# Performance work log

Hardware: AMD Instinct MI355X
Metric: run time of the kernel (lower is better)

## Reference

```python
import jax, jax.numpy as jnp
import numpy as np

S, N, L, K = 64, 8192, 512, 128  # sentences, candidate spans, max sentence length, output spans


def setup_inputs() -> dict:
    key = jax.random.key(0)
    k1, k2, k3 = jax.random.split(key, 3)
    span_scores = jax.random.normal(k1, (S, N), dtype=jnp.float32)
    starts = jax.random.randint(k2, (S, N), 0, L - 30).astype(jnp.int32)
    widths = jax.random.randint(k3, (S, N), 0, 30).astype(jnp.int32)
    ends = jnp.minimum(starts + widths, L - 1)
    return {
        "span_scores": span_scores,
        "candidate_starts": starts,
        "candidate_ends": ends,
        "num_output_spans": K,
        "max_sentence_length": L,
    }


def _select_sentence(scores, starts, ends, num_out, max_len):
    # Greedy non-crossing span selection for one sentence.
    order = jnp.argsort(-scores).astype(jnp.int32)  # descending score order
    s_sorted = starts[order]
    e_sorted = ends[order]
    pos = jnp.arange(max_len, dtype=jnp.int32)

    def step(carry, x):
        s2e, e2s, sel, n = carry  # start->latest end (init -1), end->earliest start (init L)
        i, st, en = x
        # crossing iff exists j in (st, en] with latest_end[j] > en,
        #          or j in [st, en) with earliest_start[j] < st
        crossing = jnp.any(((pos > st) & (pos <= en) & (s2e > en))
                           | ((pos >= st) & (pos < en) & (e2s < st)))
        take = jnp.logical_and(jnp.logical_not(crossing), n < num_out)
        idx = jnp.minimum(n, num_out - 1)
        sel = sel.at[idx].set(jnp.where(take, i, sel[idx]))
        s2e = jnp.where(take, s2e.at[st].max(en), s2e)
        e2s = jnp.where(take, e2s.at[en].min(st), e2s)
        n = n + take.astype(jnp.int32)
        return (s2e, e2s, sel, n), None

    init = (jnp.full((max_len,), -1, jnp.int32),
            jnp.full((max_len,), max_len, jnp.int32),
            jnp.zeros((num_out,), jnp.int32),
            jnp.int32(0))
    (s2e, e2s, sel, n), _ = jax.lax.scan(step, init, (order, s_sorted, e_sorted))
    # pad unfilled slots with the first selected index (matches torch tail-fill)
    sel = jnp.where(jnp.arange(num_out) < n, sel, sel[0])
    # sort_spans=True: order selected spans by (start, end)
    keys = starts[sel] * max_len + ends[sel]
    sel = sel[jnp.argsort(keys)]
    return sel


def reference(span_scores, candidate_starts, candidate_ends, num_output_spans, max_sentence_length):
    f = jax.vmap(lambda s, cs, ce: _select_sentence(s, cs, ce, num_output_spans, max_sentence_length))
    return f(span_scores, candidate_starts, candidate_ends).astype(jnp.int32)
```

## Files before the change

### kernel.cpp

```cpp
#include <hip/hip_runtime.h>

#define NSENT 64
#define NCAND 8192
#define LMAX  512
#define KOUT  128
#define TPB   512
#define CHUNK 1024
#define NCHUNK (NCAND / CHUNK)

#if defined(__has_builtin)
#if __has_builtin(__builtin_amdgcn_readlane)
#define READLANE(v, l) __builtin_amdgcn_readlane((unsigned)(v), (unsigned)(l))
#endif
#endif
#ifndef READLANE
#define READLANE(v, l) ((unsigned)__shfl((int)(v), (int)(l)))
#endif

__global__ __launch_bounds__(TPB) void sort_chunks_kernel(
    const float* __restrict__ scores,
    const int*   __restrict__ starts,
    const int*   __restrict__ ends,
    unsigned long long* __restrict__ ws)
{
    __shared__ unsigned long long lk[CHUNK];
    const int  bid   = blockIdx.x;
    const int  sent  = bid >> 3;
    const int  chunk = bid & 7;
    const int  tid   = threadIdx.x;
    const long gbase = (long)sent * NCAND + (long)chunk * CHUNK;

    for (int i = tid; i < CHUNK; i += TPB) {
        unsigned u  = __float_as_uint(scores[gbase + i]);
        unsigned o  = (u & 0x80000000u) ? ~u : (u | 0x80000000u);
        unsigned d  = ~o;
        unsigned st = (unsigned)starts[gbase + i];
        unsigned en = (unsigned)ends[gbase + i];
        unsigned gi = (unsigned)(chunk * CHUNK + i);
        lk[i] = ((unsigned long long)d << 32) | (gi << 18) | (st << 9) | en;
    }

    for (int k = 2; k <= CHUNK; k <<= 1) {
        for (int j = k >> 1; j > 0; j >>= 1) {
            __syncthreads();
            const int p   = tid;
            const int low = p & (j - 1);
            const int i   = ((p - low) << 1) | low;
            const int q   = i | j;
            unsigned long long a = lk[i];
            unsigned long long b = lk[q];
            bool up = ((i & k) == 0);
            if ((a > b) == up) { lk[i] = b; lk[q] = a; }
        }
    }
    __syncthreads();

    unsigned long long* wo = ws + (long)bid * CHUNK;
    for (int i = tid; i < CHUNK; i += TPB) wo[i] = lk[i];
}

__global__ __launch_bounds__(TPB) void merge_kernel(
    unsigned long long* __restrict__ ws)
{
    __shared__ __align__(16) unsigned long long keys[NCAND];
    const int sent = blockIdx.x;
    const int tid  = threadIdx.x;
    unsigned long long* wi = ws + (long)sent * NCAND;

    {
        const ulonglong2* wi2 = (const ulonglong2*)wi;
        ulonglong2* k2 = (ulonglong2*)keys;
        for (int i = tid; i < NCAND / 2; i += TPB) k2[i] = wi2[i];
    }
    __syncthreads();

    #pragma unroll
    for (int stg = 0; stg < 3; ++stg) {
        const int Lh  = CHUNK << stg;
        const int tpp = Lh >> 3;
        const int pair = tid / tpp;
        const int o    = (tid % tpp) * 16;
        const unsigned long long* A = keys + pair * (Lh * 2);
        const unsigned long long* B = A + Lh;
        int lo = (o > Lh) ? o - Lh : 0;
        int hi = (o < Lh) ? o : Lh;
        while (lo < hi) {
            int mid = (lo + hi) >> 1;
            if (A[mid] <= B[o - 1 - mid]) lo = mid + 1; else hi = mid;
        }
        int i = lo, j = o - lo;
        unsigned long long r[16];
        #pragma unroll
        for (int x = 0; x < 16; ++x) {
            bool ta = (j >= Lh) || (i < Lh && A[i] <= B[j]);
            r[x] = ta ? A[i++] : B[j++];
        }
        __syncthreads();
        unsigned long long* O = keys + pair * (Lh * 2) + o;
        #pragma unroll
        for (int x = 0; x < 16; ++x) O[x] = r[x];
        __syncthreads();
    }

    {
        const ulonglong2* k2 = (const ulonglong2*)keys;
        ulonglong2* wo2 = (ulonglong2*)wi;
        for (int i = tid; i < NCAND / 2; i += TPB) wo2[i] = k2[i];
    }
}

__global__ __launch_bounds__(128) void greedy_kernel(
    const unsigned long long* __restrict__ ws,
    int* __restrict__ out)
{
    __shared__ int TT1[5][LMAX];
    __shared__ int TT2[5][LMAX];
    __shared__ unsigned acc_list[KOUT];
    __shared__ int      n_sh;
    __shared__ unsigned mkbuf[KOUT];
    __shared__ unsigned paybuf[KOUT];

    const int sent = blockIdx.x;
    const int tid  = threadIdx.x;
    const unsigned long long* wsp = ws + (long)sent * NCAND;

    for (int i = tid; i < 5 * LMAX; i += 128) {
        (&TT1[0][0])[i] = -1;
        (&TT2[0][0])[i] = LMAX;
    }
    __syncthreads();

    if (tid < 64) {
        const int lane = tid;
        const int sidel = (lane < 31) ? lane : (lane - 31);
        const int k_m   = 31 - __clz(sidel + 1);
        const int j_m   = sidel + 1 - (1 << k_m);
        int* const rowU = (lane < 31) ? &TT1[k_m][0] : &TT2[k_m][0];

        const int NW = NCAND / 64;
        unsigned long long kv0 = wsp[lane];
        unsigned long long kv1 = wsp[64 + lane];
        int n = 0;

        for (int w = 0; w < NW && n < KOUT; ++w) {
            const unsigned pay = (unsigned)kv0;
            kv0 = kv1;
            kv1 = (w + 2 < NW) ? wsp[(long)(w + 2) * 64 + lane] : 0ull;

            const int en = (int)(pay & 511u);
            const int st = (int)((pay >> 9) & 511u);
            const int wd = en - st;

            bool alive = true;
            if (wd > 0) {
                bool cross;
                if (wd < 32) {
                    const int k   = 31 - __clz(wd);
                    const int off = 1 << k;
                    const int mx  = max(TT1[k][st + 1], TT1[k][en + 1 - off]);
                    const int mn  = min(TT2[k][st],     TT2[k][en - off]);
                    cross = (mx > en) || (mn < st);
                } else {
                    cross = false;
                    for (int j = st; j <= en; ++j)
                        cross |= ((j > st) && (TT1[0][j] > en)) ||
                                 ((j < en) && (TT2[0][j] < st));
                }
                alive = !cross;
            }

            for (;;) {
                const unsigned long long anyb = __ballot((int)alive);
                if (anyb == 0ull) break;
                const int lwin = __ffsll((long long)anyb) - 1;
                const unsigned spay = READLANE(pay, lwin);
                const int sen = (int)(spay & 511u);
                const int sst = (int)((spay >> 9) & 511u);

                if (lane == 62) acc_list[n] = spay;
                if (lane < 31)      { const int i = sst - j_m; if (i >= 0) atomicMax(&rowU[i], sen); }
                else if (lane < 62) { const int i = sen - j_m; if (i >= 0) atomicMin(&rowU[i], sst); }
                if (lane == lwin) alive = false;
                ++n;
                if (n >= KOUT) break;
                const bool c = ((st < sst) & (sst <= en) & (sen > en)) |
                               ((sst < st) & (sen >= st) & (sen < en));
                alive = alive & !c;
            }
        }
        if (lane == 0) n_sh = n;
    }
    __syncthreads();

    const int n = n_sh;
    {
        const unsigned p = (tid < n) ? acc_list[tid] : acc_list[0];
        paybuf[tid] = p;
        mkbuf[tid]  = ((p & 0x3FFFFu) << 7) | (unsigned)tid;
    }
    __syncthreads();
    {
        const unsigned mk = mkbuf[tid];
        int r = 0;
        #pragma unroll 8
        for (int t2 = 0; t2 < KOUT; ++t2) r += (mkbuf[t2] < mk) ? 1 : 0;
        out[sent * KOUT + r] = (int)(paybuf[tid] >> 18);
    }
}

__global__ __launch_bounds__(TPB) void extract_spans_mono(
    const float* __restrict__ scores,
    const int*   __restrict__ starts,
    const int*   __restrict__ ends,
    int*         __restrict__ out)
{
    __shared__ unsigned long long keys[NCAND];
    __shared__ unsigned acc_list[KOUT];
    __shared__ unsigned long long amask[TPB/64];
    __shared__ unsigned mkbuf[KOUT];
    __shared__ unsigned paybuf[KOUT];

    const int  sent = blockIdx.x;
    const int  tid  = threadIdx.x;
    const long base = (long)sent * NCAND;

    for (int i = tid; i < NCAND; i += TPB) {
        unsigned u = __float_as_uint(scores[base + i]);
        unsigned o = (u & 0x80000000u) ? ~u : (u | 0x80000000u);
        unsigned d = ~o;
        unsigned st = (unsigned)starts[base + i];
        unsigned en = (unsigned)ends[base + i];
        keys[i] = ((unsigned long long)d << 32) | ((unsigned)i << 18) | (st << 9) | en;
    }
    for (int k = 2; k <= NCAND; k <<= 1) {
        for (int j = k >> 1; j > 0; j >>= 1) {
            __syncthreads();
            for (int p = tid; p < NCAND / 2; p += TPB) {
                int low = p & (j - 1);
                int i   = ((p - low) << 1) | low;
                int q   = i | j;
                unsigned long long a = keys[i];
                unsigned long long b = keys[q];
                bool up = ((i & k) == 0);
                if ((a > b) == up) { keys[i] = b; keys[q] = a; }
            }
        }
    }
    __syncthreads();

    int  nn   = 0;
    bool done = false;
    for (int cb = 0; cb < NCAND && !done; cb += TPB) {
        const unsigned pay = (unsigned)keys[cb + tid];
        const int en = (int)(pay & 511u);
        const int st = (int)((pay >> 9) & 511u);
        bool alive = true;
        for (int a = 0; a < nn; ++a) {
            unsigned ap = acc_list[a];
            int ae = (int)(ap & 511u), as = (int)((ap >> 9) & 511u);
            if ((st < as && as <= en && ae > en) || (as < st && ae >= st && ae < en)) {
                alive = false; break;
            }
        }
        for (;;) {
            unsigned long long m = __ballot((int)alive);
            if ((tid & 63) == 0) amask[tid >> 6] = m;
            __syncthreads();
            int s = -1;
            #pragma unroll
            for (int w = 0; w < TPB / 64; ++w) {
                unsigned long long mw = amask[w];
                if (s < 0 && mw) s = (w << 6) + __ffsll((long long)mw) - 1;
            }
            __syncthreads();
            if (s < 0) break;
            unsigned spay = (unsigned)keys[cb + s];
            int sen = (int)(spay & 511u), sst = (int)((spay >> 9) & 511u);
            if (tid == 0) acc_list[nn] = spay;
            ++nn;
            if (nn == KOUT) { done = true; break; }
            if (alive) {
                alive = (tid != s) &&
                        !((st < sst && sst <= en && sen > en) ||
                          (sst < st && sen >= st && sen < en));
            }
        }
    }
    __syncthreads();
    if (tid < KOUT) {
        unsigned pay = (tid < nn) ? acc_list[tid] : acc_list[0];
        paybuf[tid] = pay;
        mkbuf[tid]  = ((pay & 0x3FFFFu) << 7) | (unsigned)tid;
    }
    __syncthreads();
    if (tid < KOUT) {
        unsigned mk = mkbuf[tid];
        int rank = 0;
        for (int t2 = 0; t2 < KOUT; ++t2)
            rank += (mkbuf[t2] < mk) ? 1 : 0;
        out[sent * KOUT + rank] = (int)(paybuf[tid] >> 18);
    }
}

extern "C" void kernel_launch(void* const* d_in, const int* in_sizes, int n_in,
                              void* d_out, int out_size, void* d_ws, size_t ws_size,
                              hipStream_t stream) {
    const float* scores = (const float*)d_in[0];
    const int*   starts = (const int*)d_in[1];
    const int*   ends   = (const int*)d_in[2];
    int*         out    = (int*)d_out;

    const size_t ws_needed = (size_t)NSENT * NCAND * sizeof(unsigned long long);
    if (ws_size >= ws_needed) {
        unsigned long long* ws = (unsigned long long*)d_ws;
        sort_chunks_kernel<<<NSENT * NCHUNK, TPB, 0, stream>>>(scores, starts, ends, ws);
        merge_kernel<<<NSENT, TPB, 0, stream>>>(ws);
        greedy_kernel<<<NSENT, 128, 0, stream>>>(ws, out);
    } else {
        extract_spans_mono<<<NSENT, TPB, 0, stream>>>(scores, starts, ends, out);
    }
}
```

Measured before the change: 124.0 us.

## Fuse merge and greedy kernels, register-resident bitonic sort, prefetch next-wave crossing tables

The chunk sort now keeps two keys per thread in registers and uses wave shuffles for small strides, a register compare for stride 512, and double-buffered LDS exchanges only for mid strides. The merge and greedy kernels are fused so the greedy scan reads merged keys straight from LDS instead of writing them to global memory and reading them back. The greedy loop also software-pipelines the next wave's sparse-table lookups and tracks crossings against newly accepted spans incrementally. The intent is to cut global round-trips, one launch, and per-step barrier and latency cost. The trade-off is higher LDS use per block and a fused block where 448 threads sit idle during the greedy phase.

After: 130.3 us. 5.1% more time.

```diff
diff --git a/kernel.cpp b/kernel.cpp
--- a/kernel.cpp
+++ b/kernel.cpp
@@ -23,50 +23,82 @@
     const int*   __restrict__ ends,
     unsigned long long* __restrict__ ws)
 {
-    __shared__ unsigned long long lk[CHUNK];
+    __shared__ unsigned long long lb[2][CHUNK];
     const int  bid   = blockIdx.x;
     const int  sent  = bid >> 3;
     const int  chunk = bid & 7;
-    const int  tid   = threadIdx.x;
+    const int  t     = threadIdx.x;
     const long gbase = (long)sent * NCAND + (long)chunk * CHUNK;
 
-    for (int i = tid; i < CHUNK; i += TPB) {
-        unsigned u  = __float_as_uint(scores[gbase + i]);
-        unsigned o  = (u & 0x80000000u) ? ~u : (u | 0x80000000u);
-        unsigned d  = ~o;
-        unsigned st = (unsigned)starts[gbase + i];
-        unsigned en = (unsigned)ends[gbase + i];
-        unsigned gi = (unsigned)(chunk * CHUNK + i);
-        lk[i] = ((unsigned long long)d << 32) | (gi << 18) | (st << 9) | en;
-    }
-
+    unsigned long long a, b;
+    {
+        unsigned u0 = __float_as_uint(scores[gbase + t]);
+        unsigned u1 = __float_as_uint(scores[gbase + t + 512]);
+        unsigned o0 = (u0 & 0x80000000u) ? ~u0 : (u0 | 0x80000000u);
+        unsigned o1 = (u1 & 0x80000000u) ? ~u1 : (u1 | 0x80000000u);
+        unsigned st0 = (unsigned)starts[gbase + t];
+        unsigned st1 = (unsigned)starts[gbase + t + 512];
+        unsigned en0 = (unsigned)ends[gbase + t];
+        unsigned en1 = (unsigned)ends[gbase + t + 512];
+        unsigned g0 = (unsigned)(chunk * CHUNK + t);
+        unsigned g1 = (unsigned)(chunk * CHUNK + t + 512);
+        a = ((unsigned long long)(~o0) << 32) | (g0 << 18) | (st0 << 9) | en0;
+        b = ((unsigned long long)(~o1) << 32) | (g1 << 18) | (st1 << 9) | en1;
+    }
+
+    int cur = 0;
     for (int k = 2; k <= CHUNK; k <<= 1) {
         for (int j = k >> 1; j > 0; j >>= 1) {
-            __syncthreads();
-            const int p   = tid;
-            const int low = p & (j - 1);
-            const int i   = ((p - low) << 1) | low;
-            const int q   = i | j;
-            unsigned long long a = lk[i];
-            unsigned long long b = lk[q];
-            bool up = ((i & k) == 0);
-            if ((a > b) == up) { lk[i] = b; lk[q] = a; }
-        }
-    }
-    __syncthreads();
+            const bool upa = ((t & k) == 0);
+            const bool upb = (((t + 512) & k) == 0);
+            if (j == 512) {
+                unsigned long long lo = (a < b) ? a : b;
+                unsigned long long hi = (a < b) ? b : a;
+                a = lo; b = hi;
+            } else if (j >= 64) {
+                lb[cur][t] = a; lb[cur][t + 512] = b;
+                __syncthreads();
+                const unsigned long long pa = lb[cur][t ^ j];
+                const unsigned long long pb = lb[cur][(t ^ j) + 512];
+                cur ^= 1;
+                const bool low = ((t & j) == 0);
+                a = ((low == upa) == (a < pa)) ? a : pa;
+                b = ((low == upb) == (b < pb)) ? b : pb;
+            } else {
+                const unsigned long long pa = __shfl_xor(a, j);
+                const unsigned long long pb = __shfl_xor(b, j);
+                const bool low = ((t & j) == 0);
+                a = ((low == upa) == (a < pa)) ? a : pa;
+                b = ((low == upb) == (b < pb)) ? b : pb;
+            }
+        }
+    }
 
     unsigned long long* wo = ws + (long)bid * CHUNK;
-    for (int i = tid; i < CHUNK; i += TPB) wo[i] = lk[i];
+    wo[t]       = a;
+    wo[t + 512] = b;
 }
 
-__global__ __launch_bounds__(TPB) void merge_kernel(
-    unsigned long long* __restrict__ ws)
+__global__ __launch_bounds__(TPB) void merge_greedy_kernel(
+    const unsigned long long* __restrict__ ws,
+    int* __restrict__ out)
 {
     __shared__ __align__(16) unsigned long long keys[NCAND];
+    __shared__ int TT1[5][LMAX];
+    __shared__ int TT2[5][LMAX];
+    __shared__ unsigned acc_list[KOUT];
+    __shared__ int      n_sh;
+    __shared__ unsigned mkbuf[KOUT];
+    __shared__ unsigned paybuf[KOUT];
+
     const int sent = blockIdx.x;
     const int tid  = threadIdx.x;
-    unsigned long long* wi = ws + (long)sent * NCAND;
-
+    const unsigned long long* wi = ws + (long)sent * NCAND;
+
+    for (int i = tid; i < 5 * LMAX; i += TPB) {
+        (&TT1[0][0])[i] = -1;
+        (&TT2[0][0])[i] = LMAX;
+    }
     {
         const ulonglong2* wi2 = (const ulonglong2*)wi;
         ulonglong2* k2 = (ulonglong2*)keys;
@@ -102,104 +134,105 @@
         __syncthreads();
     }
 
-    {
-        const ulonglong2* k2 = (const ulonglong2*)keys;
-        ulonglong2* wo2 = (ulonglong2*)wi;
-        for (int i = tid; i < NCAND / 2; i += TPB) wo2[i] = k2[i];
-    }
-}
-
-__global__ __launch_bounds__(128) void greedy_kernel(
-    const unsigned long long* __restrict__ ws,
-    int* __restrict__ out)
-{
-    __shared__ int TT1[5][LMAX];
-    __shared__ int TT2[5][LMAX];
-    __shared__ unsigned acc_list[KOUT];
-    __shared__ int      n_sh;
-    __shared__ unsigned mkbuf[KOUT];
-    __shared__ unsigned paybuf[KOUT];
-
-    const int sent = blockIdx.x;
-    const int tid  = threadIdx.x;
-    const unsigned long long* wsp = ws + (long)sent * NCAND;
-
-    for (int i = tid; i < 5 * LMAX; i += 128) {
-        (&TT1[0][0])[i] = -1;
-        (&TT2[0][0])[i] = LMAX;
-    }
-    __syncthreads();
-
     if (tid < 64) {
         const int lane = tid;
         const int sidel = (lane < 31) ? lane : (lane - 31);
         const int k_m   = 31 - __clz(sidel + 1);
         const int j_m   = sidel + 1 - (1 << k_m);
         int* const rowU = (lane < 31) ? &TT1[k_m][0] : &TT2[k_m][0];
+        const unsigned* kw = (const unsigned*)keys;
 
         const int NW = NCAND / 64;
-        unsigned long long kv0 = wsp[lane];
-        unsigned long long kv1 = wsp[64 + lane];
+        unsigned payA = kw[(0 * 64 + lane) << 1];
+        unsigned payB = kw[(1 * 64 + lane) << 1];
+        int enA = (int)(payA & 511u), stA = (int)((payA >> 9) & 511u);
+        int enB = (int)(payB & 511u), stB = (int)((payB >> 9) & 511u);
+
+        bool aliveA;
+        {
+            const int wd = enA - stA;
+            bool cross = false;
+            if (wd > 0) {
+                if (wd < 32) {
+                    const int k = 31 - __clz(wd), off = 1 << k;
+                    const int mx = max(TT1[k][stA + 1], TT1[k][enA + 1 - off]);
+                    const int mn = min(TT2[k][stA],     TT2[k][enA - off]);
+                    cross = (mx > enA) || (mn < stA);
+                } else {
+                    for (int j = stA; j <= enA; ++j)
+                        cross |= ((j > stA) && (TT1[0][j] > enA)) ||
+                                 ((j < enA) && (TT2[0][j] < stA));
+                }
+            }
+            aliveA = !cross;
+        }
+        bool aliveBacc = true;
         int n = 0;
 
         for (int w = 0; w < NW && n < KOUT; ++w) {
-            const unsigned pay = (unsigned)kv0;
-            kv0 = kv1;
-            kv1 = (w + 2 < NW) ? wsp[(long)(w + 2) * 64 + lane] : 0ull;
-
-            const int en = (int)(pay & 511u);
-            const int st = (int)((pay >> 9) & 511u);
-            const int wd = en - st;
-
-            bool alive = true;
-            if (wd > 0) {
-                bool cross;
-                if (wd < 32) {
-                    const int k   = 31 - __clz(wd);
-                    const int off = 1 << k;
-                    const int mx  = max(TT1[k][st + 1], TT1[k][en + 1 - off]);
-                    const int mn  = min(TT2[k][st],     TT2[k][en - off]);
-                    cross = (mx > en) || (mn < st);
-                } else {
-                    cross = false;
-                    for (int j = st; j <= en; ++j)
-                        cross |= ((j > st) && (TT1[0][j] > en)) ||
-                                 ((j < en) && (TT2[0][j] < st));
-                }
-                alive = !cross;
-            }
+            const int wdB = enB - stB;
+            int kB = (wdB >= 1) ? (31 - __clz(wdB)) : 0;
+            if (kB > 4) kB = 4;
+            const int offB = 1 << kB;
+            int ia = stB + 1;        if (ia > 511) ia = 511;
+            int ib = enB + 1 - offB; if (ib < 0)   ib = 0;
+            const int ic = stB;
+            int id = enB - offB;     if (id < 0)   id = 0;
+            const int tA = TT1[kB][ia], tB = TT1[kB][ib];
+            const int tC = TT2[kB][ic], tD = TT2[kB][id];
 
             for (;;) {
-                const unsigned long long anyb = __ballot((int)alive);
+                const unsigned long long anyb = __ballot((int)aliveA);
                 if (anyb == 0ull) break;
                 const int lwin = __ffsll((long long)anyb) - 1;
-                const unsigned spay = READLANE(pay, lwin);
+                const unsigned spay = READLANE(payA, lwin);
                 const int sen = (int)(spay & 511u);
                 const int sst = (int)((spay >> 9) & 511u);
 
                 if (lane == 62) acc_list[n] = spay;
                 if (lane < 31)      { const int i = sst - j_m; if (i >= 0) atomicMax(&rowU[i], sen); }
                 else if (lane < 62) { const int i = sen - j_m; if (i >= 0) atomicMin(&rowU[i], sst); }
-                if (lane == lwin) alive = false;
+                if (lane == lwin) aliveA = false;
                 ++n;
                 if (n >= KOUT) break;
-                const bool c = ((st < sst) & (sst <= en) & (sen > en)) |
-                               ((sst < st) & (sen >= st) & (sen < en));
-                alive = alive & !c;
-            }
+                const bool cA = ((stA < sst) & (sst <= enA) & (sen > enA)) |
+                                ((sst < stA) & (sen >= stA) & (sen < enA));
+                const bool cB = ((stB < sst) & (sst <= enB) & (sen > enB)) |
+                                ((sst < stB) & (sen >= stB) & (sen < enB));
+                aliveA    = aliveA    & !cA;
+                aliveBacc = aliveBacc & !cB;
+            }
+
+            bool crossB;
+            if (wdB >= 32) {
+                crossB = false;
+                for (int j = stB; j <= enB; ++j)
+                    crossB |= ((j > stB) && (TT1[0][j] > enB)) ||
+                              ((j < enB) && (TT2[0][j] < stB));
+            } else {
+                crossB = (wdB > 0) && ((max(tA, tB) > enB) || (min(tC, tD) < stB));
+            }
+            const bool aliveB = !crossB && aliveBacc;
+
+            payA = payB; stA = stB; enA = enB; aliveA = aliveB;
+            unsigned npay = 0u;
+            if (w + 2 < NW) npay = kw[((w + 2) * 64 + lane) << 1];
+            payB = npay;
+            enB = (int)(payB & 511u); stB = (int)((payB >> 9) & 511u);
+            aliveBacc = true;
         }
         if (lane == 0) n_sh = n;
     }
     __syncthreads();
 
     const int n = n_sh;
-    {
+    if (tid < KOUT) {
         const unsigned p = (tid < n) ? acc_list[tid] : acc_list[0];
         paybuf[tid] = p;
         mkbuf[tid]  = ((p & 0x3FFFFu) << 7) | (unsigned)tid;
     }
     __syncthreads();
-    {
+    if (tid < KOUT) {
         const unsigned mk = mkbuf[tid];
         int r = 0;
         #pragma unroll 8
@@ -314,8 +347,7 @@
     if (ws_size >= ws_needed) {
         unsigned long long* ws = (unsigned long long*)d_ws;
         sort_chunks_kernel<<<NSENT * NCHUNK, TPB, 0, stream>>>(scores, starts, ends, ws);
-        merge_kernel<<<NSENT, TPB, 0, stream>>>(ws);
-        greedy_kernel<<<NSENT, 128, 0, stream>>>(ws, out);
+        merge_greedy_kernel<<<NSENT, TPB, 0, stream>>>(ws, out);
     } else {
         extract_spans_mono<<<NSENT, TPB, 0, stream>>>(scores, starts, ends, out);
     }
```

## Fuse merge and greedy kernels, prefilter tail candidates in parallel

Applied to the files above, without the earlier changes.

Merges the merge-sort kernel and the greedy selection kernel into one block per sentence, so the sorted keys stay in shared memory and are not written to and re-read from global memory. After a single-wave greedy pass over the first 1024 candidates, all 512 threads check the remaining candidates in parallel against the current sparse tables. The survivors are compacted into a list with ballots and prefix popcounts, and only that list is scanned serially. This cuts one kernel launch and the serial per-window crossing checks on candidates that are already dead. In exchange it uses more shared memory per block and adds an overflow fallback that rescans from global index order when the survivor buffer fills.

Measured after the change: 121.2 us. 1.02x faster.

```diff
diff --git a/kernel.cpp b/kernel.cpp
--- a/kernel.cpp
+++ b/kernel.cpp
@@ -7,6 +7,9 @@
 #define TPB   512
 #define CHUNK 1024
 #define NCHUNK (NCAND / CHUNK)
+#define P1    1024
+#define NCH2  ((NCAND - P1) / TPB)
+#define SURV_CAP 2048
 
 #if defined(__has_builtin)
 #if __has_builtin(__builtin_amdgcn_readlane)
@@ -59,14 +62,66 @@
     for (int i = tid; i < CHUNK; i += TPB) wo[i] = lk[i];
 }
 
-__global__ __launch_bounds__(TPB) void merge_kernel(
-    unsigned long long* __restrict__ ws)
+__device__ __forceinline__ bool tt_cross(int st, int en,
+    const int (*T1)[LMAX], const int (*T2)[LMAX])
+{
+    const int wd = en - st;
+    if (wd <= 0) return false;
+    if (wd < 32) {
+        const int k   = 31 - __clz(wd);
+        const int off = 1 << k;
+        const int mx  = max(T1[k][st + 1], T1[k][en + 1 - off]);
+        const int mn  = min(T2[k][st],     T2[k][en - off]);
+        return (mx > en) || (mn < st);
+    }
+    bool cross = false;
+    for (int j = st; j <= en; ++j)
+        cross |= ((j > st) && (T1[0][j] > en)) || ((j < en) && (T2[0][j] < st));
+    return cross;
+}
+
+#define POP_WINDOW_LOOP()                                                      \
+    for (;;) {                                                                 \
+        const unsigned long long anyb = __ballot((int)alive);                  \
+        if (anyb == 0ull) break;                                               \
+        const int lwin = __ffsll((long long)anyb) - 1;                         \
+        const unsigned spay = READLANE(pay, lwin);                             \
+        const int sen = (int)(spay & 511u);                                    \
+        const int sst = (int)((spay >> 9) & 511u);                             \
+        if (lane == 62) acc_list[n] = spay;                                    \
+        if (lane < 31)      { const int ii = sst - j_m; if (ii >= 0) atomicMax(&rowU[ii], sen); } \
+        else if (lane < 62) { const int ii = sen - j_m; if (ii >= 0) atomicMin(&rowU[ii], sst); } \
+        if (lane == lwin) alive = false;                                       \
+        ++n;                                                                   \
+        if (n >= KOUT) break;                                                  \
+        const bool cR = ((st < sst) & (sst <= en) & (sen > en)) |              \
+                        ((sst < st) & (sen >= st) & (sen < en));               \
+        alive = alive & !cR;                                                   \
+    }
+
+__global__ __launch_bounds__(TPB) void merge_greedy_kernel(
+    const unsigned long long* __restrict__ ws,
+    int* __restrict__ out)
 {
     __shared__ __align__(16) unsigned long long keys[NCAND];
+    __shared__ int TT1[5][LMAX];
+    __shared__ int TT2[5][LMAX];
+    __shared__ unsigned surv[SURV_CAP];
+    __shared__ unsigned long long pmask[NCH2][8];
+    __shared__ unsigned acc_list[KOUT];
+    __shared__ int n_sh, nsurv_sh, tail_sh;
+    __shared__ unsigned mkbuf[KOUT];
+    __shared__ unsigned paybuf[KOUT];
+
     const int sent = blockIdx.x;
     const int tid  = threadIdx.x;
-    unsigned long long* wi = ws + (long)sent * NCAND;
-
+    const unsigned long long* wi = ws + (long)sent * NCAND;
+
+    for (int i = tid; i < 5 * LMAX; i += TPB) {
+        (&TT1[0][0])[i] = -1;
+        (&TT2[0][0])[i] = LMAX;
+    }
+    if (tid == 0) { n_sh = 0; nsurv_sh = 0; tail_sh = NCAND; }
     {
         const ulonglong2* wi2 = (const ulonglong2*)wi;
         ulonglong2* k2 = (ulonglong2*)keys;
@@ -102,33 +157,7 @@
         __syncthreads();
     }
 
-    {
-        const ulonglong2* k2 = (const ulonglong2*)keys;
-        ulonglong2* wo2 = (ulonglong2*)wi;
-        for (int i = tid; i < NCAND / 2; i += TPB) wo2[i] = k2[i];
-    }
-}
-
-__global__ __launch_bounds__(128) void greedy_kernel(
-    const unsigned long long* __restrict__ ws,
-    int* __restrict__ out)
-{
-    __shared__ int TT1[5][LMAX];
-    __shared__ int TT2[5][LMAX];
-    __shared__ unsigned acc_list[KOUT];
-    __shared__ int      n_sh;
-    __shared__ unsigned mkbuf[KOUT];
-    __shared__ unsigned paybuf[KOUT];
-
-    const int sent = blockIdx.x;
-    const int tid  = threadIdx.x;
-    const unsigned long long* wsp = ws + (long)sent * NCAND;
-
-    for (int i = tid; i < 5 * LMAX; i += 128) {
-        (&TT1[0][0])[i] = -1;
-        (&TT2[0][0])[i] = LMAX;
-    }
-    __syncthreads();
+    const unsigned* kw = (const unsigned*)keys;
 
     if (tid < 64) {
         const int lane = tid;
@@ -137,69 +166,96 @@
         const int j_m   = sidel + 1 - (1 << k_m);
         int* const rowU = (lane < 31) ? &TT1[k_m][0] : &TT2[k_m][0];
 
-        const int NW = NCAND / 64;
-        unsigned long long kv0 = wsp[lane];
-        unsigned long long kv1 = wsp[64 + lane];
         int n = 0;
-
-        for (int w = 0; w < NW && n < KOUT; ++w) {
-            const unsigned pay = (unsigned)kv0;
-            kv0 = kv1;
-            kv1 = (w + 2 < NW) ? wsp[(long)(w + 2) * 64 + lane] : 0ull;
-
+        for (int w = 0; w < P1 / 64 && n < KOUT; ++w) {
+            const unsigned pay = kw[(w * 64 + lane) << 1];
             const int en = (int)(pay & 511u);
             const int st = (int)((pay >> 9) & 511u);
-            const int wd = en - st;
-
-            bool alive = true;
-            if (wd > 0) {
-                bool cross;
-                if (wd < 32) {
-                    const int k   = 31 - __clz(wd);
-                    const int off = 1 << k;
-                    const int mx  = max(TT1[k][st + 1], TT1[k][en + 1 - off]);
-                    const int mn  = min(TT2[k][st],     TT2[k][en - off]);
-                    cross = (mx > en) || (mn < st);
-                } else {
-                    cross = false;
-                    for (int j = st; j <= en; ++j)
-                        cross |= ((j > st) && (TT1[0][j] > en)) ||
-                                 ((j < en) && (TT2[0][j] < st));
-                }
-                alive = !cross;
-            }
-
-            for (;;) {
-                const unsigned long long anyb = __ballot((int)alive);
-                if (anyb == 0ull) break;
-                const int lwin = __ffsll((long long)anyb) - 1;
-                const unsigned spay = READLANE(pay, lwin);
-                const int sen = (int)(spay & 511u);
-                const int sst = (int)((spay >> 9) & 511u);
-
-                if (lane == 62) acc_list[n] = spay;
-                if (lane < 31)      { const int i = sst - j_m; if (i >= 0) atomicMax(&rowU[i], sen); }
-                else if (lane < 62) { const int i = sen - j_m; if (i >= 0) atomicMin(&rowU[i], sst); }
-                if (lane == lwin) alive = false;
-                ++n;
-                if (n >= KOUT) break;
-                const bool c = ((st < sst) & (sst <= en) & (sen > en)) |
-                               ((sst < st) & (sen >= st) & (sen < en));
-                alive = alive & !c;
-            }
+            bool alive = !tt_cross(st, en, TT1, TT2);
+            POP_WINDOW_LOOP();
         }
         if (lane == 0) n_sh = n;
     }
     __syncthreads();
 
+    const int n1 = n_sh;
+    unsigned mypay[NCH2];
+    bool     myalive[NCH2];
+    if (n1 < KOUT) {
+        #pragma unroll
+        for (int c = 0; c < NCH2; ++c) {
+            const int i = P1 + c * TPB + tid;
+            const unsigned pay = kw[i << 1];
+            const int en = (int)(pay & 511u);
+            const int st = (int)((pay >> 9) & 511u);
+            const bool alive = !tt_cross(st, en, TT1, TT2);
+            mypay[c] = pay; myalive[c] = alive;
+            const unsigned long long b = __ballot((int)alive);
+            if ((tid & 63) == 0) pmask[c][tid >> 6] = b;
+        }
+    }
+    __syncthreads();
+    if (n1 < KOUT) {
+        const int myw = tid >> 6;
+        const unsigned long long below = (1ull << (tid & 63)) - 1ull;
+        unsigned run = 0;
+        #pragma unroll
+        for (int c = 0; c < NCH2; ++c) {
+            unsigned off = 0;
+            #pragma unroll
+            for (int w = 0; w < 8; ++w) {
+                const unsigned long long m = pmask[c][w];
+                if (w == myw) off = run + (unsigned)__popcll(m & below);
+                run += (unsigned)__popcll(m);
+            }
+            if (myalive[c]) {
+                if (off < SURV_CAP) surv[off] = mypay[c];
+                else atomicMin(&tail_sh, P1 + c * TPB + tid);
+            }
+        }
+        if (tid == 0) nsurv_sh = (run < SURV_CAP) ? (int)run : SURV_CAP;
+    }
+    __syncthreads();
+
+    if (tid < 64) {
+        const int lane = tid;
+        const int sidel = (lane < 31) ? lane : (lane - 31);
+        const int k_m   = 31 - __clz(sidel + 1);
+        const int j_m   = sidel + 1 - (1 << k_m);
+        int* const rowU = (lane < 31) ? &TT1[k_m][0] : &TT2[k_m][0];
+
+        int n = n_sh;
+        const int nsurv = nsurv_sh;
+        for (int s = 0; s < nsurv && n < KOUT; s += 64) {
+            const int i = s + lane;
+            const bool have = i < nsurv;
+            const unsigned pay = surv[have ? i : 0];
+            const int en = (int)(pay & 511u);
+            const int st = (int)((pay >> 9) & 511u);
+            bool alive = have && !tt_cross(st, en, TT1, TT2);
+            POP_WINDOW_LOOP();
+        }
+        for (int cb = tail_sh; cb < NCAND && n < KOUT; cb += 64) {
+            const int i = cb + lane;
+            const bool have = i < NCAND;
+            const unsigned pay = kw[(have ? i : 0) << 1];
+            const int en = (int)(pay & 511u);
+            const int st = (int)((pay >> 9) & 511u);
+            bool alive = have && !tt_cross(st, en, TT1, TT2);
+            POP_WINDOW_LOOP();
+        }
+        if (lane == 0) n_sh = n;
+    }
+    __syncthreads();
+
     const int n = n_sh;
-    {
+    if (tid < KOUT) {
         const unsigned p = (tid < n) ? acc_list[tid] : acc_list[0];
         paybuf[tid] = p;
         mkbuf[tid]  = ((p & 0x3FFFFu) << 7) | (unsigned)tid;
     }
     __syncthreads();
-    {
+    if (tid < KOUT) {
         const unsigned mk = mkbuf[tid];
         int r = 0;
         #pragma unroll 8
@@ -314,8 +370,7 @@
     if (ws_size >= ws_needed) {
         unsigned long long* ws = (unsigned long long*)d_ws;
         sort_chunks_kernel<<<NSENT * NCHUNK, TPB, 0, stream>>>(scores, starts, ends, ws);
-        merge_kernel<<<NSENT, TPB, 0, stream>>>(ws);
-        greedy_kernel<<<NSENT, 128, 0, stream>>>(ws, out);
+        merge_greedy_kernel<<<NSENT, TPB, 0, stream>>>(ws, out);
     } else {
         extract_spans_mono<<<NSENT, TPB, 0, stream>>>(scores, starts, ends, out);
     }
```
